# Kernel tuning notes

Hardware: AMD Instinct MI355X
Metric: run time of the kernel (lower is better)

Reference implementation:

```python
import jax, jax.numpy as jnp
import numpy as np

B, S, D = 2, 2048, 1024
H, HD = 16, 64


def setup_inputs() -> dict:
    key = jax.random.key(0)
    ks = jax.random.split(key, 10)
    scale = 1.0 / np.sqrt(D)
    inputs_q = jax.random.normal(ks[0], (B, S, D), dtype=jnp.float32)
    inputs_kv = jax.random.normal(ks[1], (B, S, D), dtype=jnp.float32)
    # causal mask, broadcast over batch: True = attend
    mask = jnp.broadcast_to(jnp.tril(jnp.ones((S, S), dtype=bool)), (B, S, S))
    Wq = jax.random.normal(ks[2], (D, H * HD), dtype=jnp.float32) * scale
    bq = jnp.zeros((H * HD,), dtype=jnp.float32)
    Wk = jax.random.normal(ks[3], (D, H * HD), dtype=jnp.float32) * scale
    bk = jnp.zeros((H * HD,), dtype=jnp.float32)
    Wv = jax.random.normal(ks[4], (D, H * HD), dtype=jnp.float32) * scale
    bv = jnp.zeros((H * HD,), dtype=jnp.float32)
    Wo = jax.random.normal(ks[5], (H * HD, D), dtype=jnp.float32) * scale
    bo = jnp.zeros((D,), dtype=jnp.float32)
    return {"inputs_q": inputs_q, "inputs_kv": inputs_kv, "mask": mask,
            "Wq": Wq, "bq": bq, "Wk": Wk, "bk": bk, "Wv": Wv, "bv": bv,
            "Wo": Wo, "bo": bo}


def reference(inputs_q, inputs_kv, mask, Wq, bq, Wk, bk, Wv, bv, Wo, bo):
    b, s_q, _ = inputs_q.shape
    s_k = inputs_kv.shape[1]
    # projections -> [B, S, H, HD]
    q = (inputs_q @ Wq + bq).reshape(b, s_q, H, HD)
    k = (inputs_kv @ Wk + bk).reshape(b, s_k, H, HD)
    v = (inputs_kv @ Wv + bv).reshape(b, s_k, H, HD)
    q = q / jnp.sqrt(jnp.asarray(HD, dtype=q.dtype))
    # scores: [B, H, Sq, Sk]
    attn = jnp.einsum('bqhd,bkhd->bhqk', q, k)
    m = mask[:, None, :, :]  # [B,1,Sq,Sk] broadcast over heads
    attn = jnp.where(m, attn, jnp.asarray(-1e30, dtype=attn.dtype))
    attn = jax.nn.softmax(attn, axis=-1)
    # dropout_rate = 0.0, deterministic -> identity
    out = jnp.einsum('bhqk,bkhd->bqhd', attn, v).reshape(b, s_q, H * HD)
    return out @ Wo + bo
```

## Files before the change

kernel.cpp:

```cpp
#include <hip/hip_runtime.h>

typedef __attribute__((ext_vector_type(4))) float f32x4;
typedef __attribute__((ext_vector_type(8))) short bf16x8;
typedef unsigned short u16;
typedef unsigned int u32;

#define AS1 __attribute__((address_space(1)))
#define AS3 __attribute__((address_space(3)))

#define WAITVM(N) do{ asm volatile("s_waitcnt vmcnt(" #N ")" ::: "memory"); \
                      __builtin_amdgcn_sched_barrier(0); }while(0)
#define RAWBAR    do{ __builtin_amdgcn_s_barrier();                          \
                      __builtin_amdgcn_sched_barrier(0); }while(0)

__device__ __forceinline__ float fast_exp2(float x){
  return __builtin_amdgcn_exp2f(x);
}

__device__ __forceinline__ u16 f2bf(float x){
  u32 u = __float_as_uint(x);
  u += 0x7fffu + ((u >> 16) & 1u);
  return (u16)(u >> 16);
}
__device__ __forceinline__ u16 f2bf_fast(float x){
  return (u16)((__float_as_uint(x) + 0x8000u) >> 16);
}

__global__ __launch_bounds__(256) void cvt_qkv(const float* __restrict__ s0,
                                               const float* __restrict__ s1,
                                               u16* __restrict__ d0,
                                               u16* __restrict__ d1, int n4)
{
  int i = blockIdx.x * 256 + threadIdx.x;
  if (i >= n4) return;
  const float* src = blockIdx.y ? s1 : s0;
  u16* dst = blockIdx.y ? d1 : d0;
  float4 v = reinterpret_cast<const float4*>(src)[i];
  ushort4 o;
  o.x = f2bf(v.x); o.y = f2bf(v.y); o.z = f2bf(v.z); o.w = f2bf(v.w);
  reinterpret_cast<ushort4*>(dst)[i] = o;
}

__global__ __launch_bounds__(256) void transpose_cvt4(const float* __restrict__ W0,
                                                      const float* __restrict__ W1,
                                                      const float* __restrict__ W2,
                                                      const float* __restrict__ W3,
                                                      u16* __restrict__ dst)
{
  __shared__ float tile[32][33];
  const int z = blockIdx.z;
  const float* src = z == 0 ? W0 : z == 1 ? W1 : z == 2 ? W2 : W3;
  u16* d = dst + (size_t)z * 1024 * 1024;
  int tx = threadIdx.x & 31, ty = threadIdx.x >> 5;
  int k0 = blockIdx.x * 32, n0 = blockIdx.y * 32;
  for (int r = 0; r < 4; ++r)
    tile[ty + r * 8][tx] = src[(size_t)(k0 + ty + r * 8) * 1024 + n0 + tx];
  __syncthreads();
  for (int r = 0; r < 4; ++r)
    d[(size_t)(n0 + ty + r * 8) * 1024 + k0 + tx] = f2bf(tile[tx][ty + r * 8]);
}

__global__ __launch_bounds__(256) void gemm_qkv(const u16* __restrict__ Xq,
                                                const u16* __restrict__ Xkv,
                                                const u16* __restrict__ Wt,
                                                const float* __restrict__ bq,
                                                const float* __restrict__ bk,
                                                const float* __restrict__ bv,
                                                u16* __restrict__ Qb,
                                                u16* __restrict__ Kb,
                                                u16* __restrict__ Vt,
                                                int M, int K)
{
  __shared__ u16 lA[3][128 * 32];
  __shared__ u16 lB[3][128 * 32];
  const int tid = threadIdx.x;
  const int l = tid & 63, w = tid >> 6;
  const int wr = w >> 1, wc = w & 1;
  const int bm0 = blockIdx.x * 128, bn0 = blockIdx.y * 128;
  const int seg = bn0 >> 10;
  const int nloc0 = bn0 & 1023;
  const u16* A = seg ? Xkv : Xq;
  const float* bias = seg == 0 ? bq : seg == 1 ? bk : bv;
  const float scale = seg == 0 ? 0.125f * 1.44269504089f : 1.0f;
  const int lr = l & 15, lg = (l >> 4) * 8;

#define STAGE_G(BI, KK) do{                                                   \
  _Pragma("unroll") for (int c_ = 0; c_ < 2; ++c_){                           \
    int e_ = (c_ * 256 + tid) * 8;                                            \
    int row_ = e_ >> 5, col_ = e_ & 31;                                       \
    __builtin_amdgcn_global_load_lds(                                         \
        (const AS1 u32*)(A + (size_t)(bm0 + row_) * K + (KK) * 32 + col_),    \
        (AS3 u32*)(&lA[BI][e_]), 16, 0, 0);                                   \
    __builtin_amdgcn_global_load_lds(                                         \
        (const AS1 u32*)(Wt + (size_t)(bn0 + row_) * K + (KK) * 32 + col_),   \
        (AS3 u32*)(&lB[BI][e_]), 16, 0, 0);                                   \
  }                                                                           \
}while(0)

  f32x4 acc[4][4];
#pragma unroll
  for (int m = 0; m < 4; ++m)
#pragma unroll
    for (int n = 0; n < 4; ++n) acc[m][n] = (f32x4){0.f, 0.f, 0.f, 0.f};

  STAGE_G(0, 0);
  STAGE_G(1, 1);

#pragma unroll
  for (int k = 0; k < 32; ++k){
    const int cur = k % 3;
    if (k < 30){ STAGE_G((k + 2) % 3, k + 2); WAITVM(8); }
    else if (k == 30){ WAITVM(4); }
    else { WAITVM(0); }
    RAWBAR;

    bf16x8 aF[4], bF[4];
#pragma unroll
    for (int m = 0; m < 4; ++m)
      aF[m] = *reinterpret_cast<const bf16x8*>(&lA[cur][(wr * 64 + m * 16 + lr) * 32 + lg]);
#pragma unroll
    for (int n = 0; n < 4; ++n)
      bF[n] = *reinterpret_cast<const bf16x8*>(&lB[cur][(wc * 64 + n * 16 + lr) * 32 + lg]);
    __builtin_amdgcn_s_setprio(1);
#pragma unroll
    for (int m = 0; m < 4; ++m)
#pragma unroll
      for (int n = 0; n < 4; ++n)
        acc[m][n] = __builtin_amdgcn_mfma_f32_16x16x32_bf16(aF[m], bF[n], acc[m][n], 0, 0, 0);
    __builtin_amdgcn_s_setprio(0);
    RAWBAR;
  }
#undef STAGE_G

  const int r0 = (l >> 4) * 4;
  if (seg < 2){
    u16* C = seg == 0 ? Qb : Kb;
#pragma unroll
    for (int m = 0; m < 4; ++m)
#pragma unroll
      for (int n = 0; n < 4; ++n){
        int col = nloc0 + wc * 64 + n * 16 + lr;
        float bv_ = bias[col];
#pragma unroll
        for (int r = 0; r < 4; ++r){
          int row = bm0 + wr * 64 + m * 16 + r0 + r;
          C[(size_t)row * 1024 + col] = f2bf((acc[m][n][r] + bv_) * scale);
        }
      }
  } else {
#pragma unroll
    for (int m = 0; m < 4; ++m)
#pragma unroll
      for (int n = 0; n < 4; ++n){
        int col = nloc0 + wc * 64 + n * 16 + lr;
        float bv_ = bias[col];
        int h = col >> 6, hdl = col & 63;
#pragma unroll
        for (int r = 0; r < 4; ++r){
          int row = bm0 + wr * 64 + m * 16 + r0 + r;
          int b = row >> 11, kv = row & 2047;
          size_t off = ((size_t)(b * 16 + h)) * 131072 + (size_t)hdl * 2048 + kv;
          Vt[off] = f2bf(acc[m][n][r] + bv_);
        }
      }
  }
}

__global__ __launch_bounds__(256) void gemm_out(const u16* __restrict__ A,
                                                const u16* __restrict__ Bt,
                                                const float* __restrict__ bias,
                                                float* __restrict__ Cf,
                                                int M, int N, int K)
{
  __shared__ u16 lA[64 * 32];
  __shared__ u16 lB[128 * 32];
  const int tid = threadIdx.x;
  const int l = tid & 63, w = tid >> 6;
  const int wr = w >> 1, wc = w & 1;
  const int bm0 = blockIdx.x * 64, bn0 = blockIdx.y * 128;
  const int lr = l & 15, lg = (l >> 4) * 8;

  f32x4 acc[2][4];
#pragma unroll
  for (int m = 0; m < 2; ++m)
#pragma unroll
    for (int n = 0; n < 4; ++n) acc[m][n] = (f32x4){0.f, 0.f, 0.f, 0.f};

  for (int k0 = 0; k0 < K; k0 += 32){
    {
      int e = tid * 8;
      int row = e >> 5, col = e & 31;
      __builtin_amdgcn_global_load_lds(
          (const AS1 u32*)(A + (size_t)(bm0 + row) * K + k0 + col),
          (AS3 u32*)(&lA[e]), 16, 0, 0);
    }
#pragma unroll
    for (int c = 0; c < 2; ++c){
      int e = (c * 256 + tid) * 8;
      int row = e >> 5, col = e & 31;
      __builtin_amdgcn_global_load_lds(
          (const AS1 u32*)(Bt + (size_t)(bn0 + row) * K + k0 + col),
          (AS3 u32*)(&lB[e]), 16, 0, 0);
    }
    __syncthreads();
    bf16x8 aF[2], bF[4];
#pragma unroll
    for (int m = 0; m < 2; ++m)
      aF[m] = *reinterpret_cast<const bf16x8*>(&lA[(wr * 32 + m * 16 + lr) * 32 + lg]);
#pragma unroll
    for (int n = 0; n < 4; ++n)
      bF[n] = *reinterpret_cast<const bf16x8*>(&lB[(wc * 64 + n * 16 + lr) * 32 + lg]);
    __builtin_amdgcn_s_setprio(1);
#pragma unroll
    for (int m = 0; m < 2; ++m)
#pragma unroll
      for (int n = 0; n < 4; ++n)
        acc[m][n] = __builtin_amdgcn_mfma_f32_16x16x32_bf16(aF[m], bF[n], acc[m][n], 0, 0, 0);
    __builtin_amdgcn_s_setprio(0);
    __syncthreads();
  }

  const int r0 = (l >> 4) * 4;
#pragma unroll
  for (int m = 0; m < 2; ++m)
#pragma unroll
    for (int n = 0; n < 4; ++n){
      int col = bn0 + wc * 64 + n * 16 + lr;
      float bv_ = bias[col];
#pragma unroll
      for (int r = 0; r < 4; ++r){
        int row = bm0 + wr * 32 + m * 16 + r0 + r;
        Cf[(size_t)row * N + col] = acc[m][n][r] + bv_;
      }
    }
}

__global__ __launch_bounds__(512, 2) void attn_fwd(const u16* __restrict__ Qb,
                                                   const u16* __restrict__ Kb,
                                                   const u16* __restrict__ Vt,
                                                   u16* __restrict__ AO, int S)
{
  __shared__ u16 lK[64 * 64];
  __shared__ u16 lV[64 * 64];
  __shared__ u16 lP[8][16 * 72];
  const int tid = threadIdx.x, l = tid & 63, w = tid >> 6;
  const int j = blockIdx.x;
  const int xcd = j & 7;
  const int bh = xcd * 4 + ((j >> 3) & 3);
  const int p = j >> 5;
  const int bb = bh >> 4;
  const size_t baseQK = ((size_t)bb * S) * 1024 + (bh & 15) * 64;
  const u16* gK = Kb + baseQK;
  const u16* gV = Vt + (size_t)bh * 131072;
  const int lr = l & 15, g4 = l >> 4, lg = g4 * 8;

  u16* lPw = (u16*)lP[w];
  bf16x8 ones;
#pragma unroll
  for (int i = 0; i < 8; ++i) ones[i] = (short)0x3F80;

#define STAGE_KV(T) do{                                                       \
  int row_ = tid >> 3, ch_ = tid & 7, sc_ = (ch_ ^ (row_ & 7)) * 8;           \
  __builtin_amdgcn_global_load_lds(                                           \
      (const AS1 u32*)(gK + (size_t)(64 * (T) + row_) * 1024 + sc_),          \
      (AS3 u32*)(lK + tid * 8), 16, 0, 0);                                    \
  __builtin_amdgcn_global_load_lds(                                           \
      (const AS1 u32*)(gV + (size_t)row_ * 2048 + 64 * (T) + sc_),            \
      (AS3 u32*)(lV + tid * 8), 16, 0, 0);                                    \
}while(0)

#pragma unroll
  for (int pass = 0; pass < 2; ++pass){
    const int qt = pass ? (15 - p) : p;
    const int ntb = 2 * qt + 2;
    const int q0 = qt * 128 + w * 16;

    bf16x8 qf[2];
#pragma unroll
    for (int kc = 0; kc < 2; ++kc)
      qf[kc] = *reinterpret_cast<const bf16x8*>(
          Qb + baseQK + (size_t)(q0 + lr) * 1024 + kc * 32 + lg);

    f32x4 acc_o[4], acc_l;
    acc_l = (f32x4){0.f, 0.f, 0.f, 0.f};
#pragma unroll
    for (int n = 0; n < 4; ++n) acc_o[n] = (f32x4){0.f, 0.f, 0.f, 0.f};

    for (int t = 0; t < ntb; ++t){
      STAGE_KV(t);
      __syncthreads();

      if (64 * t <= q0 + 15){
        f32x4 sA[4];
#pragma unroll
        for (int np = 0; np < 4; ++np) sA[np] = (f32x4){0.f, 0.f, 0.f, 0.f};
        __builtin_amdgcn_s_setprio(1);
#pragma unroll
        for (int kc = 0; kc < 2; ++kc)
#pragma unroll
          for (int np = 0; np < 4; ++np){
            int row = np * 16 + lr, ch = kc * 4 + g4;
            bf16x8 kf = *reinterpret_cast<const bf16x8*>(
                reinterpret_cast<const char*>(lK) + row * 128 + ((ch ^ (row & 7)) << 4));
            sA[np] = __builtin_amdgcn_mfma_f32_16x16x32_bf16(qf[kc], kf, sA[np], 0, 0, 0);
          }
        __builtin_amdgcn_s_setprio(0);

        const bool needmask = (64 * t + 63 > q0);
        if (needmask){
#pragma unroll
          for (int np = 0; np < 4; ++np){
            int kvg = 64 * t + np * 16 + lr;
#pragma unroll
            for (int r = 0; r < 4; ++r){
              int qg = q0 + g4 * 4 + r;
              float e = fast_exp2(sA[np][r]);
              lPw[(g4 * 4 + r) * 72 + np * 16 + lr] = f2bf_fast((kvg <= qg) ? e : 0.f);
            }
          }
        } else {
#pragma unroll
          for (int np = 0; np < 4; ++np)
#pragma unroll
            for (int r = 0; r < 4; ++r)
              lPw[(g4 * 4 + r) * 72 + np * 16 + lr] = f2bf_fast(fast_exp2(sA[np][r]));
        }

        bf16x8 pf[2];
#pragma unroll
        for (int kc = 0; kc < 2; ++kc)
          pf[kc] = *reinterpret_cast<const bf16x8*>(
              reinterpret_cast<const char*>(lPw) + lr * 144 + (kc * 4 + g4) * 16);
        __builtin_amdgcn_s_setprio(1);
#pragma unroll
        for (int kc = 0; kc < 2; ++kc){
          acc_l = __builtin_amdgcn_mfma_f32_16x16x32_bf16(pf[kc], ones, acc_l, 0, 0, 0);
#pragma unroll
          for (int n = 0; n < 4; ++n){
            int row = n * 16 + lr, ch = kc * 4 + g4;
            bf16x8 vf = *reinterpret_cast<const bf16x8*>(
                reinterpret_cast<const char*>(lV) + row * 128 + ((ch ^ (row & 7)) << 4));
            acc_o[n] = __builtin_amdgcn_mfma_f32_16x16x32_bf16(pf[kc], vf, acc_o[n], 0, 0, 0);
          }
        }
        __builtin_amdgcn_s_setprio(0);
      }
      __syncthreads();
    }

    float inv[4];
#pragma unroll
    for (int r = 0; r < 4; ++r) inv[r] = 1.0f / acc_l[r];
#pragma unroll
    for (int n = 0; n < 4; ++n)
#pragma unroll
      for (int r = 0; r < 4; ++r){
        int row = q0 + g4 * 4 + r;
        AO[baseQK + (size_t)row * 1024 + n * 16 + lr] = f2bf(acc_o[n][r] * inv[r]);
      }
  }
#undef STAGE_KV
}

extern "C" void kernel_launch(void* const* d_in, const int* in_sizes, int n_in,
                              void* d_out, int out_size, void* d_ws, size_t ws_size,
                              hipStream_t stream)
{
  const float* inq  = (const float*)d_in[0];
  const float* inkv = (const float*)d_in[1];
  const float* Wq = (const float*)d_in[3];
  const float* bq = (const float*)d_in[4];
  const float* Wk = (const float*)d_in[5];
  const float* bk = (const float*)d_in[6];
  const float* Wv = (const float*)d_in[7];
  const float* bv = (const float*)d_in[8];
  const float* Wo = (const float*)d_in[9];
  const float* bo = (const float*)d_in[10];
  float* out = (float*)d_out;

  const int B = 2, S = 2048, D = 1024;
  const int M = B * S;

  char* ws = (char*)d_ws;
  const size_t MB = 1024ull * 1024ull;
  u16* Xq  = (u16*)(ws + 0 * MB);
  u16* Xkv = (u16*)(ws + 8 * MB);
  u16* Wt  = (u16*)(ws + 16 * MB);
  u16* Wot = (u16*)(ws + 22 * MB);
  u16* Qb  = (u16*)(ws + 24 * MB);
  u16* Kb  = (u16*)(ws + 32 * MB);
  u16* Vtg = (u16*)(ws + 40 * MB);
  u16* AOb = (u16*)(ws + 48 * MB);

  cvt_qkv<<<dim3(M * D / 4 / 256, 2), 256, 0, stream>>>(inq, inkv, Xq, Xkv, M * D / 4);

  transpose_cvt4<<<dim3(32, 32, 4), 256, 0, stream>>>(Wq, Wk, Wv, Wo, Wt);

  gemm_qkv<<<dim3(M / 128, 3072 / 128), 256, 0, stream>>>(Xq, Xkv, Wt, bq, bk, bv,
                                                          Qb, Kb, Vtg, M, D);

  attn_fwd<<<dim3(256), 512, 0, stream>>>(Qb, Kb, Vtg, AOb, S);

  gemm_out<<<dim3(M / 64, D / 128), 256, 0, stream>>>(AOb, Wot, bo, out, M, D, D);
}
```

Before: 123.3 us.

## Multi-buffer LDS staging in output GEMM and attention to overlap loads

```diff
diff --git a/kernel.cpp b/kernel.cpp
--- a/kernel.cpp
+++ b/kernel.cpp
@@ -172,44 +172,55 @@
                                                 float* __restrict__ Cf,
                                                 int M, int N, int K)
 {
-  __shared__ u16 lA[64 * 32];
-  __shared__ u16 lB[128 * 32];
+  __shared__ u16 lA[3][64 * 32];
+  __shared__ u16 lB[3][128 * 32];
   const int tid = threadIdx.x;
   const int l = tid & 63, w = tid >> 6;
   const int wr = w >> 1, wc = w & 1;
   const int bm0 = blockIdx.x * 64, bn0 = blockIdx.y * 128;
   const int lr = l & 15, lg = (l >> 4) * 8;
 
+#define STAGE_O(BI, KK) do{                                                   \
+  {                                                                           \
+    int e_ = tid * 8;                                                         \
+    int row_ = e_ >> 5, col_ = e_ & 31;                                       \
+    __builtin_amdgcn_global_load_lds(                                         \
+        (const AS1 u32*)(A + (size_t)(bm0 + row_) * K + (KK) * 32 + col_),    \
+        (AS3 u32*)(&lA[BI][e_]), 16, 0, 0);                                   \
+  }                                                                           \
+  _Pragma("unroll") for (int c_ = 0; c_ < 2; ++c_){                           \
+    int e_ = (c_ * 256 + tid) * 8;                                            \
+    int row_ = e_ >> 5, col_ = e_ & 31;                                       \
+    __builtin_amdgcn_global_load_lds(                                         \
+        (const AS1 u32*)(Bt + (size_t)(bn0 + row_) * K + (KK) * 32 + col_),   \
+        (AS3 u32*)(&lB[BI][e_]), 16, 0, 0);                                   \
+  }                                                                           \
+}while(0)
+
   f32x4 acc[2][4];
 #pragma unroll
   for (int m = 0; m < 2; ++m)
 #pragma unroll
     for (int n = 0; n < 4; ++n) acc[m][n] = (f32x4){0.f, 0.f, 0.f, 0.f};
 
-  for (int k0 = 0; k0 < K; k0 += 32){
-    {
-      int e = tid * 8;
-      int row = e >> 5, col = e & 31;
-      __builtin_amdgcn_global_load_lds(
-          (const AS1 u32*)(A + (size_t)(bm0 + row) * K + k0 + col),
-          (AS3 u32*)(&lA[e]), 16, 0, 0);
-    }
-#pragma unroll
-    for (int c = 0; c < 2; ++c){
-      int e = (c * 256 + tid) * 8;
-      int row = e >> 5, col = e & 31;
-      __builtin_amdgcn_global_load_lds(
-          (const AS1 u32*)(Bt + (size_t)(bn0 + row) * K + k0 + col),
-          (AS3 u32*)(&lB[e]), 16, 0, 0);
-    }
-    __syncthreads();
+  STAGE_O(0, 0);
+  STAGE_O(1, 1);
+
+#pragma unroll
+  for (int k = 0; k < 32; ++k){
+    const int cur = k % 3;
+    if (k < 30){ STAGE_O((k + 2) % 3, k + 2); WAITVM(6); }
+    else if (k == 30){ WAITVM(3); }
+    else { WAITVM(0); }
+    RAWBAR;
+
     bf16x8 aF[2], bF[4];
 #pragma unroll
     for (int m = 0; m < 2; ++m)
-      aF[m] = *reinterpret_cast<const bf16x8*>(&lA[(wr * 32 + m * 16 + lr) * 32 + lg]);
+      aF[m] = *reinterpret_cast<const bf16x8*>(&lA[cur][(wr * 32 + m * 16 + lr) * 32 + lg]);
 #pragma unroll
     for (int n = 0; n < 4; ++n)
-      bF[n] = *reinterpret_cast<const bf16x8*>(&lB[(wc * 64 + n * 16 + lr) * 32 + lg]);
+      bF[n] = *reinterpret_cast<const bf16x8*>(&lB[cur][(wc * 64 + n * 16 + lr) * 32 + lg]);
     __builtin_amdgcn_s_setprio(1);
 #pragma unroll
     for (int m = 0; m < 2; ++m)
@@ -217,8 +228,9 @@
       for (int n = 0; n < 4; ++n)
         acc[m][n] = __builtin_amdgcn_mfma_f32_16x16x32_bf16(aF[m], bF[n], acc[m][n], 0, 0, 0);
     __builtin_amdgcn_s_setprio(0);
-    __syncthreads();
+    RAWBAR;
   }
+#undef STAGE_O
 
   const int r0 = (l >> 4) * 4;
 #pragma unroll
@@ -240,8 +252,8 @@
                                                    const u16* __restrict__ Vt,
                                                    u16* __restrict__ AO, int S)
 {
-  __shared__ u16 lK[64 * 64];
-  __shared__ u16 lV[64 * 64];
+  __shared__ u16 lK[2][64 * 64];
+  __shared__ u16 lV[2][64 * 64];
   __shared__ u16 lP[8][16 * 72];
   const int tid = threadIdx.x, l = tid & 63, w = tid >> 6;
   const int j = blockIdx.x;
@@ -259,14 +271,14 @@
 #pragma unroll
   for (int i = 0; i < 8; ++i) ones[i] = (short)0x3F80;
 
-#define STAGE_KV(T) do{                                                       \
+#define STAGE_KV(T, BI) do{                                                   \
   int row_ = tid >> 3, ch_ = tid & 7, sc_ = (ch_ ^ (row_ & 7)) * 8;           \
   __builtin_amdgcn_global_load_lds(                                           \
       (const AS1 u32*)(gK + (size_t)(64 * (T) + row_) * 1024 + sc_),          \
-      (AS3 u32*)(lK + tid * 8), 16, 0, 0);                                    \
+      (AS3 u32*)(&lK[BI][tid * 8]), 16, 0, 0);                                \
   __builtin_amdgcn_global_load_lds(                                           \
       (const AS1 u32*)(gV + (size_t)row_ * 2048 + 64 * (T) + sc_),            \
-      (AS3 u32*)(lV + tid * 8), 16, 0, 0);                                    \
+      (AS3 u32*)(&lV[BI][tid * 8]), 16, 0, 0);                                \
 }while(0)
 
 #pragma unroll
@@ -286,11 +298,16 @@
 #pragma unroll
     for (int n = 0; n < 4; ++n) acc_o[n] = (f32x4){0.f, 0.f, 0.f, 0.f};
 
+    int buf = 0;
+    STAGE_KV(0, 0);
     for (int t = 0; t < ntb; ++t){
-      STAGE_KV(t);
-      __syncthreads();
+      if (t + 1 < ntb){ STAGE_KV(t + 1, buf ^ 1); WAITVM(2); }
+      else            { WAITVM(0); }
+      RAWBAR;
 
       if (64 * t <= q0 + 15){
+        const u16* lKb = lK[buf];
+        const u16* lVb = lV[buf];
         f32x4 sA[4];
 #pragma unroll
         for (int np = 0; np < 4; ++np) sA[np] = (f32x4){0.f, 0.f, 0.f, 0.f};
@@ -301,7 +318,7 @@
           for (int np = 0; np < 4; ++np){
             int row = np * 16 + lr, ch = kc * 4 + g4;
             bf16x8 kf = *reinterpret_cast<const bf16x8*>(
-                reinterpret_cast<const char*>(lK) + row * 128 + ((ch ^ (row & 7)) << 4));
+                reinterpret_cast<const char*>(lKb) + row * 128 + ((ch ^ (row & 7)) << 4));
             sA[np] = __builtin_amdgcn_mfma_f32_16x16x32_bf16(qf[kc], kf, sA[np], 0, 0, 0);
           }
         __builtin_amdgcn_s_setprio(0);
@@ -339,13 +356,14 @@
           for (int n = 0; n < 4; ++n){
             int row = n * 16 + lr, ch = kc * 4 + g4;
             bf16x8 vf = *reinterpret_cast<const bf16x8*>(
-                reinterpret_cast<const char*>(lV) + row * 128 + ((ch ^ (row & 7)) << 4));
+                reinterpret_cast<const char*>(lVb) + row * 128 + ((ch ^ (row & 7)) << 4));
             acc_o[n] = __builtin_amdgcn_mfma_f32_16x16x32_bf16(pf[kc], vf, acc_o[n], 0, 0, 0);
           }
         }
         __builtin_amdgcn_s_setprio(0);
       }
-      __syncthreads();
+      RAWBAR;
+      buf ^= 1;
     }
 
     float inv[4];
```

Measured after the change: 119.0 us. 1.04x faster.
